# Kernel optimization log

Hardware: AMD Instinct MI355X
Metric: run time of the kernel (lower is better)

The kernel has to match this reference:

```python
import jax, jax.numpy as jnp
import numpy as np

B, N, DIM = 1, 100_000, 512
HEADS, DIM_HEAD, M = 8, 64, 64


def setup_inputs() -> dict:
    key = jax.random.key(0)
    ks = jax.random.split(key, 9)
    s = 0.04  # ~ kaiming-ish scale for dim=512
    return {
        "x": jax.random.normal(ks[0], (B, N, DIM), dtype=jnp.float32),
        "temperature": jnp.full((1, HEADS, 1, 1), 0.5, dtype=jnp.float32),
        "w_slice": jax.random.normal(ks[1], (HEADS * M, DIM), dtype=jnp.float32) * s,
        "b_slice": jnp.zeros((HEADS * M,), dtype=jnp.float32),
        "w1": jax.random.normal(ks[2], (DIM_HEAD, DIM), dtype=jnp.float32) * s,
        "b1": jnp.zeros((DIM_HEAD,), dtype=jnp.float32),
        "wq": jax.random.normal(ks[3], (DIM_HEAD, DIM_HEAD), dtype=jnp.float32) * 0.125,
        "wk": jax.random.normal(ks[4], (DIM_HEAD, DIM_HEAD), dtype=jnp.float32) * 0.125,
        "wv": jax.random.normal(ks[5], (DIM_HEAD, DIM_HEAD), dtype=jnp.float32) * 0.125,
        "w3": jax.random.normal(ks[6], (DIM_HEAD, DIM_HEAD), dtype=jnp.float32) * 0.125,
        "b3": jnp.zeros((DIM_HEAD,), dtype=jnp.float32),
    }


def reference(x, temperature, w_slice, b_slice, w1, b1, wq, wk, wv, w3, b3):
    b, n, c = x.shape
    # slice logits: (B,N,H*M) -> (B,H,N,M)
    logits = jnp.einsum("bnc,ec->bne", x, w_slice) + b_slice
    logits = logits.reshape(b, n, HEADS, M).transpose(0, 2, 1, 3)
    temp = jnp.clip(temperature, 0.1, 5.0)
    w = jax.nn.softmax(logits / temp, axis=-1)          # (B,H,N,M)
    d = w.sum(axis=2)                                    # (B,H,M)
    # N -> M aggregation (w^T @ x per head)
    s_raw = jnp.einsum("bhnm,bnc->bhmc", w, x)          # (B,H,M,C)
    s = jnp.einsum("bhmc,dc->bhmd", s_raw / (d[..., None] + 1e-5), w1) + b1  # (B,H,M,dh)
    q = jnp.einsum("bhmd,ed->bhme", s, wq)
    k = jnp.einsum("bhmd,ed->bhme", s, wk)
    v = jnp.einsum("bhmd,ed->bhme", s, wv)
    scale = 1.0 / jnp.sqrt(jnp.asarray(DIM_HEAD, dtype=s.dtype))
    attn = jax.nn.softmax(jnp.einsum("bhme,bhle->bhml", q, k) * scale, axis=-1)
    s_att = jnp.einsum("bhml,bhle->bhme", attn, v)      # (B,H,M,dh)
    s_out = jnp.einsum("bhme,de->bhmd", s_att, w3) + b3
    # deslice: w @ s_out -> (B,H,N,dh) -> (B,N,H*dh)
    x_out = jnp.einsum("bhnm,bhmd->bhnd", w, s_out)
    return x_out.transpose(0, 2, 1, 3).reshape(b, n, HEADS * DIM_HEAD)
```

## Files before the change

### kernel.cpp

```cpp
#include <hip/hip_runtime.h>

typedef _Float16 f16;
typedef _Float16 f16x8 __attribute__((ext_vector_type(8)));
typedef _Float16 f16x4 __attribute__((ext_vector_type(4)));
typedef float    f32x4 __attribute__((ext_vector_type(4)));

#define N_TOK   100000
#define NPAD    100032
#define NT1     1563
#define CDIM    512
#define KSTEPS  (NPAD/32)
#define K2SPL   128

#define O_WT     ((size_t)0)
#define SZ_WT    ((size_t)512*NPAD*2)
#define O_YT     (O_WT + SZ_WT)
#define SZ_YT    ((size_t)64*NPAD*2)
#define O_WFR    (O_YT + SZ_YT)
#define SZ_WFR   ((size_t)16*4*9*64*8*2)
#define O_SPP    (O_WFR + SZ_WFR)
#define SZ_SPP   ((size_t)K2SPL*32768*4)
#define O_DPP    (O_SPP + SZ_SPP)
#define SZ_DPP   ((size_t)K2SPL*512*4)
#define O_SPRE   (O_DPP + SZ_DPP)
#define SZ_SPRE  ((size_t)32768*4)
#define O_DSTD   (O_SPRE + SZ_SPRE)
#define SZ_DSTD  ((size_t)512*4)
#define O_SOUT   (O_DSTD + SZ_DSTD)
#define SZ_SOUT  ((size_t)8*64*64*2)

__global__ void k0_pack(const float* __restrict__ wsf, const float* __restrict__ w1f,
                        f16* __restrict__ wfr) {
    int c = blockIdx.x * 256 + threadIdx.x;
    int lane = c & 63, g = c >> 6;
    int u  = g % 9,  r = g / 9;
    int we = r & 3,  kg = r >> 2;
    int col = lane & 15, quad = lane >> 4;
    int k = kg * 32 + quad * 8;
    const float* src;
    if (u < 8) src = wsf + (size_t)(we*128 + u*16 + col) * CDIM + k;
    else       src = w1f + (size_t)(we*16  + col) * CDIM + k;
    float4 a = *(const float4*)(src);
    float4 b = *(const float4*)(src + 4);
    f16x8 h;
    h[0]=(f16)a.x; h[1]=(f16)a.y; h[2]=(f16)a.z; h[3]=(f16)a.w;
    h[4]=(f16)b.x; h[5]=(f16)b.y; h[6]=(f16)b.z; h[7]=(f16)b.w;
    *(f16x8*)(wfr + (size_t)c * 8) = h;
}

#define XROW 40
#define TPITCH 72
__launch_bounds__(256, 3)
__global__ void k1_slice(const float* __restrict__ x, const float* __restrict__ temperature,
                         const f16* __restrict__ wfr, const float* __restrict__ bsl,
                         f16* __restrict__ wT, f16* __restrict__ yT) {
    __shared__ f16 smem[256 * TPITCH];
    f16* lX = smem;
    f16* lT = smem;

    const int tid  = threadIdx.x;
    const int wave = tid >> 6;
    const int lane = tid & 63;
    const int quad = lane >> 4;
    const int col  = lane & 15;
    const int hgrp = blockIdx.x & 1;
    const int n0   = (blockIdx.x >> 1) * 64;
    const int h    = hgrp * 4 + wave;

    const int srow = tid >> 2, sch = tid & 3;
    int snr = n0 + srow; if (snr > N_TOK - 1) snr = N_TOK - 1;
    const float* sbase = x + (size_t)snr * CDIM + sch * 8;

    {
        float4 a = *(const float4*)(sbase);
        float4 b = *(const float4*)(sbase + 4);
        f16x8 hh;
        hh[0]=(f16)a.x; hh[1]=(f16)a.y; hh[2]=(f16)a.z; hh[3]=(f16)a.w;
        hh[4]=(f16)b.x; hh[5]=(f16)b.y; hh[6]=(f16)b.z; hh[7]=(f16)b.w;
        *(f16x8*)(&lX[srow * XROW + sch * 8]) = hh;
    }

    f32x4 acc[4][5];
    #pragma unroll
    for (int nf = 0; nf < 4; ++nf)
        #pragma unroll
        for (int u = 0; u < 5; ++u) acc[nf][u] = f32x4{0.f,0.f,0.f,0.f};

    __syncthreads();

    #pragma unroll 2
    for (int kg = 0; kg < 16; ++kg) {
        const f16* wb = wfr + ((size_t)(kg*4 + (h >> 1)) * 9 + (size_t)(h & 1) * 4) * 512
                            + (size_t)lane * 8;
        f16x8 bf[4];
        #pragma unroll
        for (int j = 0; j < 4; ++j) bf[j] = *(const f16x8*)(wb + j * 512);
        f16x8 bfy;
        if (hgrp == 0)
            bfy = *(const f16x8*)(wfr + ((size_t)(kg*4 + wave) * 9 + 8) * 512 + (size_t)lane * 8);

        float4 xa, xb;
        if (kg < 15) {
            xa = *(const float4*)(sbase + (kg + 1) * 32);
            xb = *(const float4*)(sbase + (kg + 1) * 32 + 4);
        }

        const f16* xbuf = lX + (kg & 1) * (64 * XROW);
        f16x8 af[4];
        #pragma unroll
        for (int nf = 0; nf < 4; ++nf)
            af[nf] = *(const f16x8*)(xbuf + (nf*16 + col) * XROW + quad * 8);

        #pragma unroll
        for (int nf = 0; nf < 4; ++nf)
            #pragma unroll
            for (int j = 0; j < 4; ++j)
                acc[nf][j] = __builtin_amdgcn_mfma_f32_16x16x32_f16(af[nf], bf[j], acc[nf][j], 0, 0, 0);
        if (hgrp == 0) {
            #pragma unroll
            for (int nf = 0; nf < 4; ++nf)
                acc[nf][4] = __builtin_amdgcn_mfma_f32_16x16x32_f16(af[nf], bfy, acc[nf][4], 0, 0, 0);
        }

        if (kg < 15) {
            f16x8 hh;
            hh[0]=(f16)xa.x; hh[1]=(f16)xa.y; hh[2]=(f16)xa.z; hh[3]=(f16)xa.w;
            hh[4]=(f16)xb.x; hh[5]=(f16)xb.y; hh[6]=(f16)xb.z; hh[7]=(f16)xb.w;
            *(f16x8*)(&lX[((kg + 1) & 1) * (64 * XROW) + srow * XROW + sch * 8]) = hh;
        }
        __syncthreads();
    }

    #pragma unroll
    for (int j = 0; j < 4; ++j) {
        float b = bsl[h*64 + j*16 + col];
        #pragma unroll
        for (int nf = 0; nf < 4; ++nf)
            #pragma unroll
            for (int r = 0; r < 4; ++r) acc[nf][j][r] += b;
    }
    float tv = temperature[h];
    tv = fminf(fmaxf(tv, 0.1f), 5.0f);
    const float invt = 1.0f / tv;

    #pragma unroll
    for (int nf = 0; nf < 4; ++nf) {
        const int nloc = nf*16 + quad*4;
        float mx[4];
        #pragma unroll
        for (int r = 0; r < 4; ++r) {
            float m01 = fmaxf(acc[nf][0][r], acc[nf][1][r]);
            float m23 = fmaxf(acc[nf][2][r], acc[nf][3][r]);
            mx[r] = fmaxf(m01, m23);
        }
        #pragma unroll
        for (int d = 1; d < 16; d <<= 1)
            #pragma unroll
            for (int r = 0; r < 4; ++r) mx[r] = fmaxf(mx[r], __shfl_xor(mx[r], d));
        float sm[4] = {0.f, 0.f, 0.f, 0.f};
        #pragma unroll
        for (int j = 0; j < 4; ++j)
            #pragma unroll
            for (int r = 0; r < 4; ++r) {
                float ev = __expf((acc[nf][j][r] - mx[r]) * invt);
                acc[nf][j][r] = ev;
                sm[r] += ev;
            }
        #pragma unroll
        for (int d = 1; d < 16; d <<= 1)
            #pragma unroll
            for (int r = 0; r < 4; ++r) sm[r] += __shfl_xor(sm[r], d);
        #pragma unroll
        for (int r = 0; r < 4; ++r) sm[r] = 1.0f / sm[r];
        #pragma unroll
        for (int j = 0; j < 4; ++j) {
            f16x4 pk;
            #pragma unroll
            for (int r = 0; r < 4; ++r) {
                int n = n0 + nloc + r;
                float wv = (n < N_TOK) ? acc[nf][j][r] * sm[r] : 0.0f;
                pk[r] = (f16)wv;
            }
            int e_loc = wave*64 + j*16 + col;
            *(f16x4*)(lT + (size_t)e_loc*TPITCH + nloc) = pk;
        }
        if (hgrp == 0) {
            f16x4 pk;
            #pragma unroll
            for (int r = 0; r < 4; ++r) {
                int n = n0 + nloc + r;
                pk[r] = (n < N_TOK) ? (f16)acc[nf][4][r] : (f16)0.f;
            }
            *(f16x4*)(yT + (size_t)(wave*16 + col) * NPAD + n0 + nloc) = pk;
        }
    }
    __syncthreads();

    #pragma unroll
    for (int i = 0; i < 8; ++i) {
        int id = tid + i*256;
        int e = id >> 3, p = id & 7;
        f16x8 v = *(const f16x8*)(lT + (size_t)e*TPITCH + p*8);
        *(f16x8*)(wT + (size_t)(hgrp*256 + e)*NPAD + n0 + p*8) = v;
    }
}

#define K2_LOAD(AF, BF, kss)                                                         \
    {   int nb_ = (kss)*32 + quad*8;                                                 \
        _Pragma("unroll")                                                            \
        for (int v = 0; v < 4; ++v)                                                  \
            BF[v] = *(const f16x8*)(yT + (size_t)(v*16 + col)*NPAD + nb_);           \
        _Pragma("unroll")                                                            \
        for (int u = 0; u < 2; ++u)                                                  \
            AF[u] = *(const f16x8*)(wT + (size_t)(ebase + u*16 + col)*NPAD + nb_);   \
    }
#define K2_MFMA(AF, BF)                                                              \
    {   _Pragma("unroll")                                                            \
        for (int u = 0; u < 2; ++u) {                                                \
            _Pragma("unroll")                                                        \
            for (int v = 0; v < 4; ++v)                                              \
                acc[u][v] = __builtin_amdgcn_mfma_f32_16x16x32_f16(AF[u], BF[v], acc[u][v], 0, 0, 0); \
            float s_ = 0.f;                                                          \
            _Pragma("unroll")                                                        \
            for (int j = 0; j < 8; ++j) s_ += (float)AF[u][j];                       \
            dac[u] += s_;                                                            \
        }                                                                            \
    }
__launch_bounds__(256, 4)
__global__ void k2_spre(const f16* __restrict__ wT, const f16* __restrict__ yT,
                        float* __restrict__ spp, float* __restrict__ dpp) {
    const int tid = threadIdx.x, wave = tid >> 6, lane = tid & 63;
    const int quad = lane >> 4, col = lane & 15;
    const int slot = blockIdx.x >> 2, equad = blockIdx.x & 3;
    const int ebase = equad * 128 + wave * 32;

    const int ks0 = (slot * KSTEPS) >> 7;
    const int ks1 = ((slot + 1) * KSTEPS) >> 7;

    f32x4 acc[2][4];
    float dac[2];
    #pragma unroll
    for (int u = 0; u < 2; ++u) {
        dac[u] = 0.f;
        #pragma unroll
        for (int v = 0; v < 4; ++v) acc[u][v] = f32x4{0.f,0.f,0.f,0.f};
    }

    f16x8 afA[2], bfA[4], afB[2], bfB[4];
    K2_LOAD(afA, bfA, ks0)
    int ks = ks0;
    for (; ks + 2 <= ks1; ks += 2) {
        K2_LOAD(afB, bfB, ks + 1)
        K2_MFMA(afA, bfA)
        K2_LOAD(afA, bfA, ks + 2)
        K2_MFMA(afB, bfB)
    }
    if (ks < ks1) K2_MFMA(afA, bfA)

    #pragma unroll
    for (int u = 0; u < 2; ++u) {
        dac[u] += __shfl_xor(dac[u], 16);
        dac[u] += __shfl_xor(dac[u], 32);
    }
    if (quad == 0) {
        #pragma unroll
        for (int u = 0; u < 2; ++u)
            dpp[slot*512 + ebase + u*16 + col] = dac[u];
    }
    float* dst = spp + (size_t)slot * 32768 + (size_t)equad * 8192;
    #pragma unroll
    for (int u = 0; u < 2; ++u)
        #pragma unroll
        for (int v = 0; v < 4; ++v)
            *(f32x4*)(dst + (size_t)((wave*2 + u)*4 + v)*256 + (size_t)lane*4) = acc[u][v];
}

__global__ void k2r_reduce(const float* __restrict__ spp, const float* __restrict__ dpp,
                           float* __restrict__ spre, float* __restrict__ dstd) {
    int i = blockIdx.x*256 + threadIdx.x;
    float s = 0.f;
    for (int p = 0; p < K2SPL; ++p) s += spp[(size_t)p*32768 + i];
    int r = i & 3, L = (i >> 2) & 63, v = (i >> 8) & 3, g = (i >> 10) & 7, eq = (i >> 13) & 3;
    int e = eq*128 + (g >> 1)*32 + (g & 1)*16 + (L >> 4)*4 + r;
    int d = v*16 + (L & 15);
    spre[e*64 + d] = s;
    if (i < 512) {
        float tt = 0.f;
        for (int p = 0; p < K2SPL; ++p) tt += dpp[p*512 + i];
        dstd[i] = tt;
    }
}

__global__ void k3_attn(const float* __restrict__ spre, const float* __restrict__ dstd,
                        const float* __restrict__ b1, const float* __restrict__ wq,
                        const float* __restrict__ wk, const float* __restrict__ wv,
                        const float* __restrict__ w3, const float* __restrict__ b3,
                        f16* __restrict__ sout) {
    __shared__ float wa[64][65], wb[64][65], wc[64][65];
    __shared__ float ss[64][65], kk[64][65], vv[64][65];
    __shared__ float qq[16][65], sc[16][65];
    const int h = blockIdx.x >> 2, ms = blockIdx.x & 3, tid = threadIdx.x;

    for (int i = tid; i < 4096; i += 256) {
        int r = i >> 6, c = i & 63;
        wa[r][c] = wq[i];
        wb[r][c] = wk[i];
        wc[r][c] = wv[i];
        ss[r][c] = spre[h*4096 + i] / (dstd[h*64 + r] + 1e-5f) + b1[c];
    }
    __syncthreads();

    #pragma unroll
    for (int it = 0; it < 16; ++it) {
        int m = it*4 + (tid >> 6), e = tid & 63;
        float ak = 0.f, av = 0.f;
        #pragma unroll 8
        for (int d = 0; d < 64; ++d) {
            float sv = ss[m][d];
            ak += sv * wb[e][d];
            av += sv * wc[e][d];
        }
        kk[m][e] = ak; vv[m][e] = av;
    }
    #pragma unroll
    for (int it = 0; it < 4; ++it) {
        int ml = it*4 + (tid >> 6), e = tid & 63;
        float aq = 0.f;
        #pragma unroll 8
        for (int d = 0; d < 64; ++d) aq += ss[ms*16 + ml][d] * wa[e][d];
        qq[ml][e] = aq;
    }
    __syncthreads();

    for (int i = tid; i < 4096; i += 256) wa[i >> 6][i & 63] = w3[i];
    #pragma unroll
    for (int it = 0; it < 4; ++it) {
        int ml = it*4 + (tid >> 6), l = tid & 63;
        float a = 0.f;
        #pragma unroll 8
        for (int e = 0; e < 64; ++e) a += qq[ml][e] * kk[l][e];
        sc[ml][l] = a * 0.125f;
    }
    __syncthreads();

    if (tid < 16) {
        int ml = tid;
        float mx = -1e30f;
        #pragma unroll 8
        for (int l = 0; l < 64; ++l) mx = fmaxf(mx, sc[ml][l]);
        float sm = 0.f;
        #pragma unroll 8
        for (int l = 0; l < 64; ++l) { float ev = __expf(sc[ml][l] - mx); sc[ml][l] = ev; sm += ev; }
        float rs = 1.0f / sm;
        #pragma unroll 8
        for (int l = 0; l < 64; ++l) sc[ml][l] *= rs;
    }
    __syncthreads();

    #pragma unroll
    for (int it = 0; it < 4; ++it) {
        int ml = it*4 + (tid >> 6), e = tid & 63;
        float a = 0.f;
        #pragma unroll 8
        for (int l = 0; l < 64; ++l) a += sc[ml][l] * vv[l][e];
        qq[ml][e] = a;
    }
    __syncthreads();

    #pragma unroll
    for (int it = 0; it < 4; ++it) {
        int d = it*16 + (tid >> 4), ml = tid & 15;
        float a = b3[d];
        #pragma unroll 8
        for (int e = 0; e < 64; ++e) a += qq[ml][e] * wa[d][e];
        sout[(h*64 + d)*64 + ms*16 + ml] = (f16)a;
    }
}

#define K4PITCH 36
__launch_bounds__(256, 4)
__global__ void k4_deslice(const f16* __restrict__ wT, const f16* __restrict__ sout,
                           float* __restrict__ out) {
    __shared__ f16 ldsW[512 * K4PITCH];
    const int tid = threadIdx.x, wave = tid >> 6, lane = tid & 63;
    const int quad = lane >> 4, col = lane & 15;

    const int bid = blockIdx.x;
    const int xcd = bid & 7, idx = bid >> 3;
    const int q = KSTEPS >> 3, r = KSTEPS & 7;
    const int swz = (xcd < r ? xcd*(q+1) : r*(q+1) + (xcd - r)*q) + idx;
    const int n0 = swz * 32;

    #pragma unroll
    for (int i = 0; i < 8; ++i) {
        int id = tid + i*256;
        int e = id >> 2, p = id & 3;
        f16x8 v = *(const f16x8*)(wT + (size_t)e*NPAD + n0 + p*8);
        *(f16x8*)(ldsW + (size_t)e*K4PITCH + p*8) = v;
    }
    __syncthreads();

    f32x4 acc[2][2][4];
    #pragma unroll
    for (int hh = 0; hh < 2; ++hh)
        #pragma unroll
        for (int t = 0; t < 2; ++t)
            #pragma unroll
            for (int v = 0; v < 4; ++v) acc[hh][t][v] = f32x4{0.f,0.f,0.f,0.f};

    #pragma unroll
    for (int hh = 0; hh < 2; ++hh) {
        int h = wave*2 + hh;
        #pragma unroll
        for (int ks = 0; ks < 2; ++ks) {
            f16x8 af[2], bf[4];
            #pragma unroll
            for (int t = 0; t < 2; ++t) {
                f16x8 a;
                #pragma unroll
                for (int j = 0; j < 8; ++j)
                    a[j] = ldsW[(size_t)(h*64 + ks*32 + quad*8 + j)*K4PITCH + t*16 + col];
                af[t] = a;
            }
            #pragma unroll
            for (int v = 0; v < 4; ++v)
                bf[v] = *(const f16x8*)(sout + (size_t)(h*64 + v*16 + col)*64 + ks*32 + quad*8);
            #pragma unroll
            for (int t = 0; t < 2; ++t)
                #pragma unroll
                for (int v = 0; v < 4; ++v)
                    acc[hh][t][v] = __builtin_amdgcn_mfma_f32_16x16x32_f16(af[t], bf[v], acc[hh][t][v], 0, 0, 0);
        }
    }

    #pragma unroll
    for (int hh = 0; hh < 2; ++hh) {
        int h = wave*2 + hh;
        #pragma unroll
        for (int t = 0; t < 2; ++t)
            #pragma unroll
            for (int v = 0; v < 4; ++v)
                #pragma unroll
                for (int r2 = 0; r2 < 4; ++r2) {
                    int n = n0 + t*16 + quad*4 + r2;
                    if (n < N_TOK)
                        out[(size_t)n*512 + h*64 + v*16 + col] = acc[hh][t][v][r2];
                }
    }
}

extern "C" void kernel_launch(void* const* d_in, const int* in_sizes, int n_in,
                              void* d_out, int out_size, void* d_ws, size_t ws_size,
                              hipStream_t stream) {
    const float* x           = (const float*)d_in[0];
    const float* temperature = (const float*)d_in[1];
    const float* w_slice     = (const float*)d_in[2];
    const float* b_slice     = (const float*)d_in[3];
    const float* w1          = (const float*)d_in[4];
    const float* b1          = (const float*)d_in[5];
    const float* wq          = (const float*)d_in[6];
    const float* wk          = (const float*)d_in[7];
    const float* wv          = (const float*)d_in[8];
    const float* w3          = (const float*)d_in[9];
    const float* b3          = (const float*)d_in[10];
    float* out = (float*)d_out;
    char*  ws  = (char*)d_ws;

    f16*   wT    = (f16*)(ws + O_WT);
    f16*   yT    = (f16*)(ws + O_YT);
    f16*   wfr   = (f16*)(ws + O_WFR);
    float* spp   = (float*)(ws + O_SPP);
    float* dpp   = (float*)(ws + O_DPP);
    float* spre  = (float*)(ws + O_SPRE);
    float* dstd  = (float*)(ws + O_DSTD);
    f16*   sout  = (f16*)(ws + O_SOUT);

    k0_pack<<<144, 256, 0, stream>>>(w_slice, w1, wfr);
    k1_slice<<<NT1*2, 256, 0, stream>>>(x, temperature, wfr, b_slice, wT, yT);
    k2_spre<<<K2SPL*4, 256, 0, stream>>>(wT, yT, spp, dpp);
    k2r_reduce<<<128, 256, 0, stream>>>(spp, dpp, spre, dstd);
    k3_attn<<<32, 256, 0, stream>>>(spre, dstd, b1, wq, wk, wv, w3, b3, sout);
    k4_deslice<<<KSTEPS, 256, 0, stream>>>(wT, sout, out);
}
```

Before: 579.7 us.

## Swizzle k1 block order and stage k4 output through LDS for vectorized stores

Result: faster. 563.0 us (-2.9%).

```diff
diff --git a/kernel.cpp b/kernel.cpp
--- a/kernel.cpp
+++ b/kernel.cpp
@@ -63,8 +63,13 @@
     const int lane = tid & 63;
     const int quad = lane >> 4;
     const int col  = lane & 15;
-    const int hgrp = blockIdx.x & 1;
-    const int n0   = (blockIdx.x >> 1) * 64;
+
+    const int b = blockIdx.x;
+    int nt, hg;
+    if (b < 3120) { nt = (b >> 4) * 8 + (b & 7); hg = (b >> 3) & 1; }
+    else          { nt = 1560 + ((b - 3120) >> 1); hg = (b - 3120) & 1; }
+    const int hgrp = hg;
+    const int n0   = nt * 64;
     const int h    = hgrp * 4 + wave;
 
     const int srow = tid >> 2, sch = tid & 3;
@@ -73,10 +78,10 @@
 
     {
         float4 a = *(const float4*)(sbase);
-        float4 b = *(const float4*)(sbase + 4);
+        float4 bb = *(const float4*)(sbase + 4);
         f16x8 hh;
         hh[0]=(f16)a.x; hh[1]=(f16)a.y; hh[2]=(f16)a.z; hh[3]=(f16)a.w;
-        hh[4]=(f16)b.x; hh[5]=(f16)b.y; hh[6]=(f16)b.z; hh[7]=(f16)b.w;
+        hh[4]=(f16)bb.x; hh[5]=(f16)bb.y; hh[6]=(f16)bb.z; hh[7]=(f16)bb.w;
         *(f16x8*)(&lX[srow * XROW + sch * 8]) = hh;
     }
 
@@ -133,11 +138,11 @@
 
     #pragma unroll
     for (int j = 0; j < 4; ++j) {
-        float b = bsl[h*64 + j*16 + col];
+        float bb = bsl[h*64 + j*16 + col];
         #pragma unroll
         for (int nf = 0; nf < 4; ++nf)
             #pragma unroll
-            for (int r = 0; r < 4; ++r) acc[nf][j][r] += b;
+            for (int r = 0; r < 4; ++r) acc[nf][j][r] += bb;
     }
     float tv = temperature[h];
     tv = fminf(fmaxf(tv, 0.1f), 5.0f);
@@ -381,7 +386,10 @@
 __launch_bounds__(256, 4)
 __global__ void k4_deslice(const f16* __restrict__ wT, const f16* __restrict__ sout,
                            float* __restrict__ out) {
-    __shared__ f16 ldsW[512 * K4PITCH];
+    __shared__ __align__(16) char lmem[512 * K4PITCH * 2];
+    f16*   ldsW = (f16*)lmem;
+    float* ldsO = (float*)lmem;
+
     const int tid = threadIdx.x, wave = tid >> 6, lane = tid & 63;
     const int quad = lane >> 4, col = lane & 15;
 
@@ -434,18 +442,28 @@
     }
 
     #pragma unroll
-    for (int hh = 0; hh < 2; ++hh) {
-        int h = wave*2 + hh;
-        #pragma unroll
-        for (int t = 0; t < 2; ++t)
+    for (int p = 0; p < 2; ++p) {
+        __syncthreads();
+        #pragma unroll
+        for (int hh = 0; hh < 2; ++hh) {
+            int h = wave*2 + hh;
             #pragma unroll
             for (int v = 0; v < 4; ++v)
                 #pragma unroll
-                for (int r2 = 0; r2 < 4; ++r2) {
-                    int n = n0 + t*16 + quad*4 + r2;
-                    if (n < N_TOK)
-                        out[(size_t)n*512 + h*64 + v*16 + col] = acc[hh][t][v][r2];
-                }
+                for (int r2 = 0; r2 < 4; ++r2)
+                    ldsO[(size_t)(quad*4 + r2)*516 + h*64 + v*16 + col] = acc[hh][p][v][r2];
+        }
+        __syncthreads();
+        #pragma unroll
+        for (int it = 0; it < 8; ++it) {
+            int id = tid + it*256;
+            int row = id >> 7, ch = id & 127;
+            int n = n0 + p*16 + row;
+            if (n < N_TOK) {
+                float4 v4 = *(const float4*)(ldsO + (size_t)row*516 + ch*4);
+                *(float4*)(out + (size_t)n*512 + ch*4) = v4;
+            }
+        }
     }
 }
 
```
